# Kernel optimization log

Hardware: AMD Instinct MI355X
Metric: run time of the kernel (lower is better)

The kernel has to match this reference:

```python
import jax, jax.numpy as jnp
import numpy as np

EMB = 1280
MD = 200
N = 20000
E = 200000
LN_EPS = 1e-5


def _layer_norm(x, g, b):
    mu = jnp.mean(x, axis=-1, keepdims=True)
    var = jnp.mean((x - mu) ** 2, axis=-1, keepdims=True)
    return (x - mu) * jax.lax.rsqrt(var + LN_EPS) * g + b


def _gat_conv(x, edge_index, edge_attr, W, We, a_src, a_dst, a_edge, bias, heads, C):
    """PyG GATConv (bias-free lin, edge_dim, add_self_loops with fill='mean')."""
    n = x.shape[0]
    src, dst = edge_index[0], edge_index[1]
    # self-loop edge_attr = mean of incoming edge_attr per dst node (0 if none)
    cnt = jax.ops.segment_sum(jnp.ones((edge_attr.shape[0],), x.dtype), dst, n)
    s = jax.ops.segment_sum(edge_attr, dst, n)
    loop_attr = jnp.where(cnt[:, None] > 0, s / jnp.maximum(cnt, 1.0)[:, None], 0.0)
    loop = jnp.arange(n)
    src = jnp.concatenate([src, loop])
    dst = jnp.concatenate([dst, loop])
    ea = jnp.concatenate([edge_attr, loop_attr], axis=0)
    h = (x @ W).reshape(n, heads, C)                      # [N,H,C]
    al_s = jnp.einsum('nhc,hc->nh', h, a_src)
    al_d = jnp.einsum('nhc,hc->nh', h, a_dst)
    eh = (ea @ We).reshape(-1, heads, C)                  # [E+N,H,C]
    al_e = jnp.einsum('ehc,hc->eh', eh, a_edge)
    alpha = jax.nn.leaky_relu(al_s[src] + al_d[dst] + al_e, 0.2)
    amax = jax.ops.segment_max(alpha, dst, n)
    amax = jnp.where(jnp.isfinite(amax), amax, 0.0)
    ex = jnp.exp(alpha - amax[dst])
    denom = jax.ops.segment_sum(ex, dst, n)
    w = ex / (denom[dst] + 1e-16)                         # segment softmax over dst
    out = jax.ops.segment_sum(h[src] * w[:, :, None], dst, n)
    return out.reshape(n, heads * C) + bias


def _forward(x, edge_index, edge_attr,
             ca_qw, ca_qb, ca_kw, ca_kb, ca_vw, ca_vb, ca_ow, ca_ob,
             g0_w, g0_ew, g0_as, g0_ad, g0_ae, g0_b, ln0_g, ln0_b,
             g1_w, g1_ew, g1_as, g1_ad, g1_ae, g1_b, ln1_g, ln1_b,
             g2_w, g2_ew, g2_as, g2_ad, g2_ae, g2_b, ln2_g, ln2_b,
             cls_w1, cls_b1, cls_w2, cls_b2):
    xe = x[:, :EMB]
    md = x[0, EMB:]
    # CrossAttention: single md vector -> K,V are [1,hidden]
    Q = xe @ ca_qw + ca_qb                                # [N,hid]
    K = md @ ca_kw + ca_kb                                # [hid]
    V = md @ ca_vw + ca_vb                                # [hid]
    scores = (Q @ K) / jnp.sqrt(jnp.asarray(Q.shape[-1], Q.dtype))  # [N]
    wts = jax.nn.softmax(scores, axis=0)[:, None]         # softmax over nodes
    attended = wts * V[None, :]                           # [N,hid]
    h = attended @ ca_ow + ca_ob + xe                     # [N,EMB]

    h = _gat_conv(h, edge_index, edge_attr, g0_w, g0_ew, g0_as, g0_ad, g0_ae, g0_b, 4, 256)
    h = jax.nn.relu(_layer_norm(h, ln0_g, ln0_b))
    h = _gat_conv(h, edge_index, edge_attr, g1_w, g1_ew, g1_as, g1_ad, g1_ae, g1_b, 4, 256)
    h = jax.nn.relu(_layer_norm(h, ln1_g, ln1_b))
    h = _gat_conv(h, edge_index, edge_attr, g2_w, g2_ew, g2_as, g2_ad, g2_ae, g2_b, 1, 256)
    h = jax.nn.relu(_layer_norm(h, ln2_g, ln2_b))

    g = jnp.mean(h, axis=0, keepdims=True)                # [1,256]
    g = jax.nn.relu(g @ cls_w1 + cls_b1)
    return g @ cls_w2 + cls_b2                            # [1,2]


def setup_inputs() -> dict:
    key = jax.random.key(0)
    ks = jax.random.split(key, 64)
    i = [0]
    def nrm(shape, scale=0.05):
        i[0] += 1
        return jax.random.normal(ks[i[0]], shape, jnp.float32) * scale
    inp = {}
    inp['x'] = nrm((N, EMB + MD), 1.0)
    inp['edge_index'] = jax.random.randint(ks[60], (2, E), 0, N, jnp.int64 if jax.config.read('jax_enable_x64') else jnp.int32)
    inp['edge_attr'] = jax.random.uniform(ks[61], (E, 1), jnp.float32)
    inp.update(ca_qw=nrm((EMB, 256)), ca_qb=jnp.zeros((256,), jnp.float32),
               ca_kw=nrm((MD, 256)), ca_kb=jnp.zeros((256,), jnp.float32),
               ca_vw=nrm((MD, 256)), ca_vb=jnp.zeros((256,), jnp.float32),
               ca_ow=nrm((256, EMB)), ca_ob=jnp.zeros((EMB,), jnp.float32))
    inp.update(g0_w=nrm((EMB, 1024)), g0_ew=nrm((1, 1024)), g0_as=nrm((4, 256)),
               g0_ad=nrm((4, 256)), g0_ae=nrm((4, 256)), g0_b=jnp.zeros((1024,), jnp.float32),
               ln0_g=jnp.ones((1024,), jnp.float32), ln0_b=jnp.zeros((1024,), jnp.float32))
    inp.update(g1_w=nrm((1024, 1024)), g1_ew=nrm((1, 1024)), g1_as=nrm((4, 256)),
               g1_ad=nrm((4, 256)), g1_ae=nrm((4, 256)), g1_b=jnp.zeros((1024,), jnp.float32),
               ln1_g=jnp.ones((1024,), jnp.float32), ln1_b=jnp.zeros((1024,), jnp.float32))
    inp.update(g2_w=nrm((1024, 256)), g2_ew=nrm((1, 256)), g2_as=nrm((1, 256)),
               g2_ad=nrm((1, 256)), g2_ae=nrm((1, 256)), g2_b=jnp.zeros((256,), jnp.float32),
               ln2_g=jnp.ones((256,), jnp.float32), ln2_b=jnp.zeros((256,), jnp.float32))
    inp.update(cls_w1=nrm((256, 128)), cls_b1=jnp.zeros((128,), jnp.float32),
               cls_w2=nrm((128, 2)), cls_b2=jnp.zeros((2,), jnp.float32))
    return inp


def reference(x, edge_index, edge_attr,
              ca_qw, ca_qb, ca_kw, ca_kb, ca_vw, ca_vb, ca_ow, ca_ob,
              g0_w, g0_ew, g0_as, g0_ad, g0_ae, g0_b, ln0_g, ln0_b,
              g1_w, g1_ew, g1_as, g1_ad, g1_ae, g1_b, ln1_g, ln1_b,
              g2_w, g2_ew, g2_as, g2_ad, g2_ae, g2_b, ln2_g, ln2_b,
              cls_w1, cls_b1, cls_w2, cls_b2):
    return _forward(x, edge_index, edge_attr,
                    ca_qw, ca_qb, ca_kw, ca_kb, ca_vw, ca_vb, ca_ow, ca_ob,
                    g0_w, g0_ew, g0_as, g0_ad, g0_ae, g0_b, ln0_g, ln0_b,
                    g1_w, g1_ew, g1_as, g1_ad, g1_ae, g1_b, ln1_g, ln1_b,
                    g2_w, g2_ew, g2_as, g2_ad, g2_ae, g2_b, ln2_g, ln2_b,
                    cls_w1, cls_b1, cls_w2, cls_b2)
```

## Files before the change

kernel.cpp:

```cpp
#include <hip/hip_runtime.h>
#include <hip/hip_bf16.h>
#include <math.h>

#define N_NODES 20000
#define N_EDGES 200000
#define XROW    1480

typedef __attribute__((ext_vector_type(8))) _Float16 f16x8;
typedef __attribute__((ext_vector_type(8))) unsigned short u16x8;
typedef __attribute__((ext_vector_type(4))) float f32x4v;

__device__ __forceinline__ float wsum(float v){
#pragma unroll
  for (int o=32;o>0;o>>=1) v += __shfl_down(v,o);
  return v;
}
__device__ __forceinline__ float wmax(float v){
#pragma unroll
  for (int o=32;o>0;o>>=1) v = fmaxf(v,__shfl_down(v,o));
  return v;
}
__device__ __forceinline__ float wsum_all(float v){
#pragma unroll
  for (int o=32;o>0;o>>=1) v += __shfl_xor(v,o);
  return v;
}
__device__ __forceinline__ float wmax_all(float v){
#pragma unroll
  for (int o=32;o>0;o>>=1) v = fmaxf(v,__shfl_xor(v,o));
  return v;
}

__device__ __forceinline__ unsigned short f2hu(float f){
  _Float16 h = (_Float16)f;
  return __builtin_bit_cast(unsigned short, h);
}
__device__ __forceinline__ float hu2f(unsigned short u){
  return (float)__builtin_bit_cast(_Float16, u);
}

__device__ __forceinline__ void async_copy16(void* lds, const void* g){
  __builtin_amdgcn_global_load_lds((const __attribute__((address_space(1))) void*)g,
                                   (__attribute__((address_space(3))) void*)lds, 16, 0, 0);
}

__global__ void edge_count_kernel(const int* __restrict__ ei, const float* __restrict__ ea,
                                  int* __restrict__ cnt, float* __restrict__ easum, int E){
  int e = blockIdx.x*256 + threadIdx.x;
  if (e >= E) return;
  int dst = ei[E + e];
  atomicAdd(&cnt[dst], 1);
  atomicAdd(&easum[dst], ea[e]);
}

__launch_bounds__(1024)
__global__ void scan_kernel(const int* __restrict__ cnt, const float* __restrict__ easum,
                            int* __restrict__ off, float* __restrict__ loop_attr, int n){
  __shared__ int buf[1024];
  const int PER = (N_NODES + 1023)/1024;
  int t = threadIdx.x;
  int base = t*PER;
  int local[PER];
  int s = 0;
#pragma unroll
  for (int k=0;k<PER;k++){
    int i = base + k;
    int v = (i<n)? cnt[i] : 0;
    local[k] = v;
    s += v;
  }
  buf[t] = s;
  __syncthreads();
  for (int d2=1; d2<1024; d2<<=1){
    int tv = (t>=d2)? buf[t-d2] : 0;
    __syncthreads();
    buf[t] += tv;
    __syncthreads();
  }
  int run = buf[t] - s;
#pragma unroll
  for (int k=0;k<PER;k++){
    int i = base + k;
    if (i < n){
      off[i] = run;
      int v = local[k];
      loop_attr[i] = (v>0) ? easum[i]/(float)v : 0.f;
      run += v;
    }
  }
  if (t == 1023) off[n] = buf[1023];
}

__global__ void edge_fill_kernel(const int* __restrict__ ei, const float* __restrict__ ea,
                                 const int* __restrict__ off, int* __restrict__ fill,
                                 int* __restrict__ csr_src, float* __restrict__ csr_ea, int E){
  int e = blockIdx.x*256 + threadIdx.x;
  if (e >= E) return;
  int dst = ei[E + e];
  int pos = off[dst] + atomicAdd(&fill[dst], 1);
  csr_src[pos] = ei[e];
  csr_ea[pos]  = ea[e];
}

__global__ void wt_f16_kernel(const float* __restrict__ W, int K, int N,
                              unsigned short* __restrict__ Wt){
  __shared__ float tile[32][33];
  int k0 = blockIdx.x*32, n0 = blockIdx.y*32;
  int tx = threadIdx.x & 31, ty = threadIdx.x >> 5;
  for (int r=ty; r<32; r+=8) tile[r][tx] = W[(size_t)(k0+r)*N + n0+tx];
  __syncthreads();
  for (int r=ty; r<32; r+=8){
    float w = tile[tx][r];
    Wt[(size_t)(n0+r)*K + k0+tx] = f2hu(w);
  }
}

__global__ void kv_kernel(const float* __restrict__ x,
                          const float* __restrict__ kw, const float* __restrict__ kb,
                          const float* __restrict__ vw, const float* __restrict__ vb,
                          float* __restrict__ Kv, float* __restrict__ Vv){
  int j = threadIdx.x;
  float ka = kb[j], va = vb[j];
  for (int k=0;k<200;k++){
    float m = x[1280+k];
    ka = fmaf(m, kw[k*256+j], ka);
    va = fmaf(m, vw[k*256+j], va);
  }
  Kv[j]=ka; Vv[j]=va;
}

__global__ void qkvo_kernel(const float* __restrict__ qw, const float* __restrict__ ow,
                            const float* __restrict__ Kv, const float* __restrict__ Vv,
                            float* __restrict__ qK, float* __restrict__ Vo){
  int idx = blockIdx.x*256 + threadIdx.x;
  if (idx < 1280){
    float a=0;
    for (int j=0;j<256;j++) a = fmaf(qw[idx*256+j], Kv[j], a);
    qK[idx]=a;
  } else if (idx < 2560){
    int j = idx-1280;
    float a=0;
    for (int i=0;i<256;i++) a = fmaf(Vv[i], ow[(size_t)i*1280+j], a);
    Vo[j]=a;
  }
}

__global__ void obw_kernel(const float* __restrict__ ob, const float* __restrict__ Vo,
                           const float* __restrict__ W, float* __restrict__ obW, float* __restrict__ VoW){
  int j = blockIdx.x*256 + threadIdx.x;
  float a=0,b=0;
  for (int i=0;i<1280;i++){
    float w = W[(size_t)i*1024+j];
    a = fmaf(ob[i], w, a);
    b = fmaf(Vo[i], w, b);
  }
  obW[j]=a; VoW[j]=b;
}

__launch_bounds__(256)
__global__ void xh_scores_kernel(const float* __restrict__ x, const float* __restrict__ qK,
                                 unsigned short* __restrict__ xh, float* __restrict__ scores, int n){
  __shared__ float qs[1280];
  int t = threadIdx.x;
  for (int i=t;i<1280;i+=256) qs[i]=qK[i];
  __syncthreads();
  int wid = t>>6, lane = t&63;
  int node = blockIdx.x*4 + wid;
  if (node >= n) return;
  const float* xr = x + (size_t)node*XROW;
  unsigned short* orow = xh + (size_t)node*1280;
  float acc = 0.f;
#pragma unroll
  for (int it=0; it<5; it++){
    int c4 = it*64 + lane;
    float4 v = *(const float4*)(xr + c4*4);
    ushort4 o;
    o.x = f2hu(v.x); o.y = f2hu(v.y); o.z = f2hu(v.z); o.w = f2hu(v.w);
    *(ushort4*)(orow + c4*4) = o;
    acc = fmaf(v.x, qs[c4*4+0], acc);
    acc = fmaf(v.y, qs[c4*4+1], acc);
    acc = fmaf(v.z, qs[c4*4+2], acc);
    acc = fmaf(v.w, qs[c4*4+3], acc);
  }
  acc = wsum(acc);
  if (lane==0) scores[node] = acc;
}

__launch_bounds__(1024)
__global__ void softmax_nodes(const float* __restrict__ scores, float* __restrict__ wts, int n){
  __shared__ float red[16];
  int t = threadIdx.x, lane=t&63, wid=t>>6;
  float m = -INFINITY;
  for (int i=t;i<n;i+=1024) m = fmaxf(m, scores[i]);
  m = wmax(m);
  if (lane==0) red[wid]=m;
  __syncthreads();
  if (t==0){ float r=red[0]; for (int k=1;k<16;k++) r=fmaxf(r,red[k]); red[0]=r; }
  __syncthreads();
  float M = red[0];
  __syncthreads();
  float z=0;
  for (int i=t;i<n;i+=1024) z += __expf((scores[i]-M)*(1.f/16.f));
  z = wsum(z);
  if (lane==0) red[wid]=z;
  __syncthreads();
  if (t==0){ float r=0; for (int k=0;k<16;k++) r+=red[k]; red[0]=r; }
  __syncthreads();
  float invZ = 1.f/red[0];
  for (int i=t;i<n;i+=1024) wts[i] = __expf((scores[i]-M)*(1.f/16.f))*invZ;
}

__launch_bounds__(512,2)
__global__ void gemm256_f16(const unsigned short* __restrict__ A,
                            const unsigned short* __restrict__ B,
                            unsigned short* __restrict__ C, int M, int N, int K,
                            const float* __restrict__ addCol,
                            const float* __restrict__ vCol,
                            const float* __restrict__ wRow,
                            const float* __restrict__ a_src,
                            const float* __restrict__ a_dst,
                            float* __restrict__ als,
                            float* __restrict__ ald,
                            const float* __restrict__ We,
                            const float* __restrict__ a_edge,
                            float* __restrict__ we)
{
  __shared__ short lds[2*32768];

  const int ntc = N >> 8;
  const int sh  = (ntc==4)?2:((ntc==2)?1:0);
  const int g   = blockIdx.y >> sh;
  const int nt  = blockIdx.y & (ntc - 1);
  const int band = blockIdx.x + (g << 3);
  if (band * 256 >= M) return;

  const int t = threadIdx.x;
  const int w = t>>6, l = t&63;
  const int bm = band*256, bn = nt*256;
  const int wrh = w>>2;
  const int wcl = (w&3)*64;
  const int q4 = l>>4, m16 = l&15;

  f32x4v acc[8][4];
#pragma unroll
  for (int i=0;i<8;i++)
#pragma unroll
    for (int j=0;j<4;j++) acc[i][j] = (f32x4v){0.f,0.f,0.f,0.f};

  const unsigned short *pA00,*pA01,*pA10,*pA11,*pB00,*pB01,*pB10,*pB11;
  int lA00,lA01,lA10,lA11,lB00,lB01,lB10,lB11;
  {
#pragma unroll
    for (int half=0; half<2; half++){
#pragma unroll
      for (int q=0; q<2; q++){
        int p  = (w*2+q)*64 + l;
        int r  = p>>3, pc = p&7;
        int kc = (pc ^ (r&7))*8;
        int rowA = bm + half*128 + r; if (rowA > M-1) rowA = M-1;
        int rowB = bn + half*128 + r;
        const unsigned short* ap = A + (size_t)rowA*K + kc;
        const unsigned short* bp = B + (size_t)rowB*K + kc;
        int la = half*8192 + (w*2+q)*512;
        int lb = 16384 + la;
        if (half==0 && q==0){ pA00=ap; pB00=bp; lA00=la; lB00=lb; }
        if (half==0 && q==1){ pA01=ap; pB01=bp; lA01=la; lB01=lb; }
        if (half==1 && q==0){ pA10=ap; pB10=bp; lA10=la; lB10=lb; }
        if (half==1 && q==1){ pA11=ap; pB11=bp; lA11=la; lB11=lb; }
      }
    }
  }

  const int nk = K >> 6;

  {
    short* b0 = lds;
    async_copy16(b0 + lA00, pA00); async_copy16(b0 + lA01, pA01);
    async_copy16(b0 + lA10, pA10); async_copy16(b0 + lA11, pA11);
    async_copy16(b0 + lB00, pB00); async_copy16(b0 + lB01, pB01);
    async_copy16(b0 + lB10, pB10); async_copy16(b0 + lB11, pB11);
    asm volatile("s_waitcnt vmcnt(0)" ::: "memory");
    __builtin_amdgcn_sched_barrier(0);
    __builtin_amdgcn_s_barrier();
    __builtin_amdgcn_sched_barrier(0);
  }

  for (int kt = 0; kt < nk; ++kt){
    short* cur = lds + (kt&1)*32768;
    short* nxt = lds + ((kt+1)&1)*32768;
    const bool pre = (kt+1 < nk);
    const size_t kofs = (size_t)(kt+1)*64;

    f16x8 bf[4];
#pragma unroll
    for (int ph = 0; ph < 4; ++ph){
      const int ks = ph >> 1, ih = ph & 1;
      const int c  = ks*4 + q4;
      f16x8 af[4];
#pragma unroll
      for (int ii=0; ii<4; ii++){
        int rl = (ih*4+ii)*16 + m16;
        af[ii] = *(const f16x8*)&cur[ wrh*8192 + rl*64 + ((c ^ (rl&7))*8) ];
      }
      if (ih == 0){
#pragma unroll
        for (int j=0;j<4;j++){
          int rb = wcl + j*16 + m16;
          bf[j] = *(const f16x8*)&cur[ 16384 + rb*64 + ((c ^ (rb&7))*8) ];
        }
      }
      if (pre){
        if (ph == 0){
          async_copy16(nxt + lA00, pA00 + kofs); async_copy16(nxt + lA01, pA01 + kofs);
          async_copy16(nxt + lA10, pA10 + kofs); async_copy16(nxt + lA11, pA11 + kofs);
        } else if (ph == 1){
          async_copy16(nxt + lB00, pB00 + kofs); async_copy16(nxt + lB01, pB01 + kofs);
          async_copy16(nxt + lB10, pB10 + kofs); async_copy16(nxt + lB11, pB11 + kofs);
        }
      }
      __builtin_amdgcn_sched_barrier(0);
      __builtin_amdgcn_s_barrier();
      asm volatile("s_waitcnt lgkmcnt(0)" ::: "memory");
      __builtin_amdgcn_sched_barrier(0);

      __builtin_amdgcn_s_setprio(1);
#pragma unroll
      for (int ii=0; ii<4; ii++)
#pragma unroll
        for (int j=0; j<4; j++)
          acc[ih*4+ii][j] = __builtin_amdgcn_mfma_f32_16x16x32_f16(af[ii], bf[j], acc[ih*4+ii][j], 0,0,0);
      __builtin_amdgcn_s_setprio(0);
      __builtin_amdgcn_sched_barrier(0);
      if (ph == 3){
        asm volatile("s_waitcnt vmcnt(0)" ::: "memory");
        __builtin_amdgcn_sched_barrier(0);
      }
      __builtin_amdgcn_s_barrier();
      __builtin_amdgcn_sched_barrier(0);
    }
  }

  __syncthreads();
  float* sred = (float*)lds;
  float* dred = sred + 1024;
  const int bandc = w & 3;

  float asv[4], adv[4];
#pragma unroll
  for (int j=0;j<4;j++){
    int n = bn + wcl + j*16 + m16;
    asv[j] = a_src[n];
    adv[j] = a_dst[n];
  }
#pragma unroll
  for (int i=0;i<8;i++){
#pragma unroll
    for (int r=0;r<4;r++){
      int rloc = wrh*128 + i*16 + q4*4 + r;
      int m = bm + rloc;
      float wrow = addCol ? wRow[m < M ? m : M-1] : 0.f;
      float vj[4];
#pragma unroll
      for (int j=0;j<4;j++){
        int n = bn + wcl + j*16 + m16;
        float v = acc[i][j][r];
        if (addCol) v += addCol[n] + wrow*vCol[n];
        vj[j] = v;
      }
      if (m < M){
        unsigned short* crow = C + (size_t)m*N;
#pragma unroll
        for (int j=0;j<4;j++) crow[bn + wcl + j*16 + m16] = f2hu(vj[j]);
      }
      float s = vj[0]*asv[0] + vj[1]*asv[1] + vj[2]*asv[2] + vj[3]*asv[3];
      float d = vj[0]*adv[0] + vj[1]*adv[1] + vj[2]*adv[2] + vj[3]*adv[3];
#pragma unroll
      for (int o=1;o<16;o<<=1){ s += __shfl_xor(s,o); d += __shfl_xor(d,o); }
      if (m16 == 0){
        sred[bandc*256 + rloc] = s;
        dred[bandc*256 + rloc] = d;
      }
    }
  }
  __syncthreads();
  if (t < 256){
    int m = bm + t;
    if (m < M){
      float s = sred[t] + sred[256+t] + sred[512+t] + sred[768+t];
      float d = dred[t] + dred[256+t] + dred[512+t] + dred[768+t];
      als[(size_t)m*ntc + nt] = s;
      ald[(size_t)m*ntc + nt] = d;
    }
  }
  if (band == 0 && nt == 0 && w < ntc){
    float4 a = ((const float4*)(We + w*256))[l];
    float4 b = ((const float4*)(a_edge + w*256))[l];
    float v = a.x*b.x + a.y*b.y + a.z*b.z + a.w*b.w;
    v = wsum(v);
    if (l==0) we[w]=v;
  }
}

__launch_bounds__(256)
__global__ void gemm_f16(const unsigned short* __restrict__ A,
                         const unsigned short* __restrict__ B,
                         unsigned short* __restrict__ C, int M, int N, int K,
                         const float* __restrict__ addCol,
                         const float* __restrict__ vCol,
                         const float* __restrict__ wRow,
                         const float* __restrict__ a_src,
                         const float* __restrict__ a_dst,
                         float* __restrict__ alsp,
                         float* __restrict__ aldp)
{
  __shared__ short lds[2*2*128*64];

  const int ntc = N >> 7;
  const int sh  = __popc(ntc - 1);
  const int g   = blockIdx.y >> sh;
  const int nt  = blockIdx.y & (ntc - 1);
  const int band = blockIdx.x + (g << 3);
  if (band * 128 >= M) return;

  const int t = threadIdx.x;
  const int w = t>>6, l = t&63;
  const int bm = band*128, bn = nt*128;
  const int wr = (w>>1)*64, wc = (w&1)*64;
  const int half = w & 1;

  f32x4v acc[4][4];
#pragma unroll
  for (int i=0;i<4;i++)
#pragma unroll
    for (int j=0;j<4;j++) acc[i][j] = (f32x4v){0.f,0.f,0.f,0.f};

  const unsigned short* Ap[4]; const unsigned short* Bp[4];
  int ldsOff[4];
#pragma unroll
  for (int q=0;q<4;q++){
    int p  = (w*4+q)*64 + l;
    int r  = p>>3, pc = p&7;
    int kc = (pc ^ (r&7))*8;
    int rowA = bm + r; if (rowA > M-1) rowA = M-1;
    Ap[q] = A + (size_t)rowA*K + kc;
    Bp[q] = B + (size_t)(bn+r)*K + kc;
    ldsOff[q] = (w*4+q)*64*8;
  }

  const int nsteps = K >> 6;

#pragma unroll
  for (int q=0;q<4;q++) async_copy16(lds + ldsOff[q],        Ap[q]);
#pragma unroll
  for (int q=0;q<4;q++) async_copy16(lds + 8192 + ldsOff[q], Bp[q]);

  const int q4 = l>>4, m16 = l&15;

  for (int ks0=0; ks0<nsteps; ++ks0){
    short* curb = lds + (ks0&1)*16384;

    if (ks0+1 < nsteps){
      short* nxt = lds + ((ks0+1)&1)*16384;
      const int k0n = (ks0+1)*64;
#pragma unroll
      for (int q=0;q<4;q++) async_copy16(nxt + ldsOff[q],        Ap[q] + k0n);
#pragma unroll
      for (int q=0;q<4;q++) async_copy16(nxt + 8192 + ldsOff[q], Bp[q] + k0n);
      asm volatile("s_waitcnt vmcnt(8)" ::: "memory");
    } else {
      asm volatile("s_waitcnt vmcnt(0)" ::: "memory");
    }
    __builtin_amdgcn_sched_barrier(0);
    __builtin_amdgcn_s_barrier();
    __builtin_amdgcn_sched_barrier(0);

    __builtin_amdgcn_s_setprio(1);
#pragma unroll
    for (int ks=0; ks<2; ks++){
      f16x8 af[4], bf[4];
      const int c = ks*4 + q4;
#pragma unroll
      for (int i=0;i<4;i++){
        int ra = wr + i*16 + m16;
        af[i] = *(const f16x8*)&curb[ra*64 + ((c ^ (ra&7))*8)];
        int rb = wc + i*16 + m16;
        bf[i] = *(const f16x8*)&curb[8192 + rb*64 + ((c ^ (rb&7))*8)];
      }
#pragma unroll
      for (int i=0;i<4;i++)
#pragma unroll
        for (int j=0;j<4;j++)
          acc[i][j] = __builtin_amdgcn_mfma_f32_16x16x32_f16(af[i], bf[j], acc[i][j], 0,0,0);
    }
    __builtin_amdgcn_s_setprio(0);
    __builtin_amdgcn_sched_barrier(0);
    __builtin_amdgcn_s_barrier();
    __builtin_amdgcn_sched_barrier(0);
  }

  float* sred = (float*)lds;
  float* dred = sred + 256;
  float asv[4], adv[4];
#pragma unroll
  for (int j=0;j<4;j++){
    int n = bn + wc + j*16 + m16;
    asv[j] = a_src[n];
    adv[j] = a_dst[n];
  }
#pragma unroll
  for (int i=0;i<4;i++){
#pragma unroll
    for (int r=0;r<4;r++){
      int rloc = wr + i*16 + q4*4 + r;
      int m = bm + rloc;
      float wrow = addCol ? wRow[m < M ? m : M-1] : 0.f;
      float vj[4];
#pragma unroll
      for (int j=0;j<4;j++){
        int n = bn + wc + j*16 + m16;
        float v = acc[i][j][r];
        if (addCol) v += addCol[n] + wrow*vCol[n];
        vj[j] = v;
      }
      if (m < M){
        unsigned short* crow = C + (size_t)m*N;
#pragma unroll
        for (int j=0;j<4;j++) crow[bn + wc + j*16 + m16] = f2hu(vj[j]);
      }
      float s = vj[0]*asv[0] + vj[1]*asv[1] + vj[2]*asv[2] + vj[3]*asv[3];
      float d = vj[0]*adv[0] + vj[1]*adv[1] + vj[2]*adv[2] + vj[3]*adv[3];
#pragma unroll
      for (int o=1;o<16;o<<=1){ s += __shfl_xor(s,o); d += __shfl_xor(d,o); }
      if (m16 == 0){
        sred[half*128 + rloc] = s;
        dred[half*128 + rloc] = d;
      }
    }
  }
  __syncthreads();
  if (t < 128){
    int m = bm + t;
    if (m < M){
      alsp[(size_t)nt*M + m] = sred[t] + sred[128+t];
      aldp[(size_t)nt*M + m] = dred[t] + dred[128+t];
    }
  }
}

__global__ void als_combine(const float* __restrict__ alsp, const float* __restrict__ aldp,
                            float* __restrict__ als, float* __restrict__ ald, int M, int H,
                            const float* __restrict__ We, const float* __restrict__ a_edge,
                            float* __restrict__ we){
  if (blockIdx.x == 0){
    int wid = threadIdx.x>>6, lane = threadIdx.x&63;
    if (wid < H){
      const float4* w4 = (const float4*)(We + wid*256);
      const float4* a4 = (const float4*)(a_edge + wid*256);
      float4 a = w4[lane], b = a4[lane];
      float v = a.x*b.x + a.y*b.y + a.z*b.z + a.w*b.w;
      v = wsum(v);
      if (lane==0) we[wid]=v;
    }
  }
  int idx = blockIdx.x*256 + threadIdx.x;
  if (idx >= M*H) return;
  int m = idx / H, hh = idx - m*H;
  als[idx] = alsp[(size_t)(2*hh)*M + m] + alsp[(size_t)(2*hh+1)*M + m];
  ald[idx] = aldp[(size_t)(2*hh)*M + m] + aldp[(size_t)(2*hh+1)*M + m];
}

template<int H>
__launch_bounds__(256)
__global__ void gat_agg_ln_wave(const unsigned short* __restrict__ hmat,
                           const float* __restrict__ als, const float* __restrict__ ald,
                           const int* __restrict__ off, const int* __restrict__ csr_src,
                           const float* __restrict__ csr_ea, const float* __restrict__ loop_attr,
                           const float* __restrict__ we,
                           const float* __restrict__ bias,
                           const float* __restrict__ ln_g, const float* __restrict__ ln_b,
                           float* __restrict__ outf, unsigned short* __restrict__ outb, int n)
{
  constexpr int OUT = 256*H;
  constexpr int CPL = OUT/64;
  const int wv = threadIdx.x>>6, lane = threadIdx.x&63;
  const int i = blockIdx.x*4 + wv;
  __shared__ float wbuf_s[4][64*H];
  __shared__ int   sbuf_s[4][64];
  if (i >= n) return;
  float* wbuf = wbuf_s[wv];
  int*   sbuf = sbuf_s[wv];

  const int begin = off[i];
  const int deg   = off[i+1]-begin;
  const int S     = deg + 1;

  float aldi[H], wei[H];
#pragma unroll
  for (int hh=0;hh<H;hh++){ aldi[hh]=ald[(size_t)i*H+hh]; wei[hh]=we[hh]; }
  const float lea = loop_attr[i];

  const int head = (lane*CPL) >> 8;
  const int c0   = lane*CPL;
  float acc[CPL];
#pragma unroll
  for (int c=0;c<CPL;c++) acc[c]=0.f;

  if (S <= 64){
    int src = i; float ev = lea;
    if (lane < deg){ src = csr_src[begin+lane]; ev = csr_ea[begin+lane]; }
    const bool act = lane < S;
    sbuf[lane] = src;

    if constexpr (CPL==16){
      u16x8 a0r0,a0r1,a1r0,a1r1;
      {
        const unsigned short* r0p = hmat + (size_t)sbuf[0]*OUT + c0;
        a0r0 = *(const u16x8*)r0p; a0r1 = *(const u16x8*)(r0p+8);
        a1r0 = a0r0; a1r1 = a0r1;
        if (S > 1){
          const unsigned short* r1p = hmat + (size_t)sbuf[1]*OUT + c0;
          a1r0 = *(const u16x8*)r1p; a1r1 = *(const u16x8*)(r1p+8);
        }
      }
      float a[H];
#pragma unroll
      for (int hh=0;hh<H;hh++){
        float v = als[(size_t)src*H+hh] + aldi[hh] + ev*wei[hh];
        a[hh] = v>0.f ? v : 0.2f*v;
      }
#pragma unroll
      for (int hh=0;hh<H;hh++){
        float M = wmax_all(act ? a[hh] : -INFINITY);
        float e = act ? __expf(a[hh]-M) : 0.f;
        float Z = wsum_all(e);
        wbuf[lane*H+hh] = e / (Z + 1e-16f);
      }
      int j = 0;
      for (; j+2<S; j+=2){
        u16x8 n0r0,n0r1,n1r0,n1r1;
        {
          const unsigned short* rp = hmat + (size_t)sbuf[j+2]*OUT + c0;
          n0r0 = *(const u16x8*)rp; n0r1 = *(const u16x8*)(rp+8);
          n1r0 = n0r0; n1r1 = n0r1;
          if (j+3 < S){
            const unsigned short* rq = hmat + (size_t)sbuf[j+3]*OUT + c0;
            n1r0 = *(const u16x8*)rq; n1r1 = *(const u16x8*)(rq+8);
          }
        }
        float w0 = wbuf[j*H+head], w1 = wbuf[(j+1)*H+head];
#pragma unroll
        for (int c=0;c<8;c++){
          acc[c]   = fmaf(w0, hu2f(a0r0[c]), acc[c]);
          acc[8+c] = fmaf(w0, hu2f(a0r1[c]), acc[8+c]);
        }
#pragma unroll
        for (int c=0;c<8;c++){
          acc[c]   = fmaf(w1, hu2f(a1r0[c]), acc[c]);
          acc[8+c] = fmaf(w1, hu2f(a1r1[c]), acc[8+c]);
        }
        a0r0=n0r0; a0r1=n0r1; a1r0=n1r0; a1r1=n1r1;
      }
      {
        float w0 = wbuf[j*H+head];
#pragma unroll
        for (int c=0;c<8;c++){
          acc[c]   = fmaf(w0, hu2f(a0r0[c]), acc[c]);
          acc[8+c] = fmaf(w0, hu2f(a0r1[c]), acc[8+c]);
        }
        if (j+1 < S){
          float w1 = wbuf[(j+1)*H+head];
#pragma unroll
          for (int c=0;c<8;c++){
            acc[c]   = fmaf(w1, hu2f(a1r0[c]), acc[c]);
            acc[8+c] = fmaf(w1, hu2f(a1r1[c]), acc[8+c]);
          }
        }
      }
    } else {
      ushort4 a0, a1;
      {
        a0 = *(const ushort4*)(hmat + (size_t)sbuf[0]*OUT + c0);
        a1 = a0;
        if (S > 1) a1 = *(const ushort4*)(hmat + (size_t)sbuf[1]*OUT + c0);
      }
      float a[H];
#pragma unroll
      for (int hh=0;hh<H;hh++){
        float v = als[(size_t)src*H+hh] + aldi[hh] + ev*wei[hh];
        a[hh] = v>0.f ? v : 0.2f*v;
      }
#pragma unroll
      for (int hh=0;hh<H;hh++){
        float M = wmax_all(act ? a[hh] : -INFINITY);
        float e = act ? __expf(a[hh]-M) : 0.f;
        float Z = wsum_all(e);
        wbuf[lane*H+hh] = e / (Z + 1e-16f);
      }
      int j = 0;
      for (; j+2<S; j+=2){
        ushort4 n0, n1;
        n0 = *(const ushort4*)(hmat + (size_t)sbuf[j+2]*OUT + c0);
        n1 = n0;
        if (j+3 < S) n1 = *(const ushort4*)(hmat + (size_t)sbuf[j+3]*OUT + c0);
        float w0 = wbuf[j*H+head], w1 = wbuf[(j+1)*H+head];
        acc[0]=fmaf(w0,hu2f(a0.x),acc[0]); acc[1]=fmaf(w0,hu2f(a0.y),acc[1]);
        acc[2]=fmaf(w0,hu2f(a0.z),acc[2]); acc[3]=fmaf(w0,hu2f(a0.w),acc[3]);
        acc[0]=fmaf(w1,hu2f(a1.x),acc[0]); acc[1]=fmaf(w1,hu2f(a1.y),acc[1]);
        acc[2]=fmaf(w1,hu2f(a1.z),acc[2]); acc[3]=fmaf(w1,hu2f(a1.w),acc[3]);
        a0=n0; a1=n1;
      }
      {
        float w0 = wbuf[j*H+head];
        acc[0]=fmaf(w0,hu2f(a0.x),acc[0]); acc[1]=fmaf(w0,hu2f(a0.y),acc[1]);
        acc[2]=fmaf(w0,hu2f(a0.z),acc[2]); acc[3]=fmaf(w0,hu2f(a0.w),acc[3]);
        if (j+1 < S){
          float w1 = wbuf[(j+1)*H+head];
          acc[0]=fmaf(w1,hu2f(a1.x),acc[0]); acc[1]=fmaf(w1,hu2f(a1.y),acc[1]);
          acc[2]=fmaf(w1,hu2f(a1.z),acc[2]); acc[3]=fmaf(w1,hu2f(a1.w),acc[3]);
        }
      }
    }
  } else {
    float rm[H];
#pragma unroll
    for (int hh=0;hh<H;hh++) rm[hh] = -INFINITY;
    for (int s=lane; s<S; s+=64){
      int src = (s<deg)? csr_src[begin+s] : i;
      float ev = (s<deg)? csr_ea[begin+s] : lea;
#pragma unroll
      for (int hh=0;hh<H;hh++){
        float v = als[(size_t)src*H+hh] + aldi[hh] + ev*wei[hh];
        v = v>0.f? v : 0.2f*v;
        rm[hh] = fmaxf(rm[hh], v);
      }
    }
    float M[H], es[H];
#pragma unroll
    for (int hh=0;hh<H;hh++){ M[hh]=wmax_all(rm[hh]); es[hh]=0.f; }
    for (int s=lane; s<S; s+=64){
      int src = (s<deg)? csr_src[begin+s] : i;
      float ev = (s<deg)? csr_ea[begin+s] : lea;
#pragma unroll
      for (int hh=0;hh<H;hh++){
        float v = als[(size_t)src*H+hh] + aldi[hh] + ev*wei[hh];
        v = v>0.f? v : 0.2f*v;
        es[hh] += __expf(v - M[hh]);
      }
    }
    float invZ[H];
#pragma unroll
    for (int hh=0;hh<H;hh++) invZ[hh] = 1.f/(wsum_all(es[hh]) + 1e-16f);
    for (int cb=0; cb<S; cb+=64){
      int m = min(64, S-cb);
      int s = cb + lane;
      if (s < S){
        int src = (s<deg)? csr_src[begin+s] : i;
        float ev = (s<deg)? csr_ea[begin+s] : lea;
        sbuf[lane] = src;
#pragma unroll
        for (int hh=0;hh<H;hh++){
          float v = als[(size_t)src*H+hh] + aldi[hh] + ev*wei[hh];
          v = v>0.f? v : 0.2f*v;
          wbuf[lane*H+hh] = __expf(v - M[hh]) * invZ[hh];
        }
      }
      for (int j=0;j<m;j++){
        int sj = sbuf[j];
        float wj = wbuf[j*H+head];
        const unsigned short* row = hmat + (size_t)sj*OUT + c0;
        if constexpr (CPL==16){
          u16x8 r0 = *(const u16x8*)(row);
          u16x8 r1 = *(const u16x8*)(row+8);
#pragma unroll
          for (int c=0;c<8;c++){
            acc[c]   = fmaf(wj, hu2f(r0[c]), acc[c]);
            acc[8+c] = fmaf(wj, hu2f(r1[c]), acc[8+c]);
          }
        } else {
          ushort4 r = *(const ushort4*)(row);
          acc[0]=fmaf(wj,hu2f(r.x),acc[0]); acc[1]=fmaf(wj,hu2f(r.y),acc[1]);
          acc[2]=fmaf(wj,hu2f(r.z),acc[2]); acc[3]=fmaf(wj,hu2f(r.w),acc[3]);
        }
      }
    }
  }

  float vals[CPL];
  float ls=0.f;
#pragma unroll
  for (int c=0;c<CPL;c+=4){
    float4 b4 = *(const float4*)(bias + c0 + c);
    vals[c]=acc[c]+b4.x; vals[c+1]=acc[c+1]+b4.y; vals[c+2]=acc[c+2]+b4.z; vals[c+3]=acc[c+3]+b4.w;
    ls += vals[c]+vals[c+1]+vals[c+2]+vals[c+3];
  }
  float mu = wsum_all(ls) * (1.f/OUT);
  float lv=0.f;
#pragma unroll
  for (int c=0;c<CPL;c++){ float d=vals[c]-mu; lv += d*d; }
  float inv = rsqrtf(wsum_all(lv)*(1.f/OUT) + 1e-5f);

  if (outb){
    if constexpr (CPL==16){
#pragma unroll
      for (int c=0;c<CPL;c+=8){
        u16x8 o;
#pragma unroll
        for (int k=0;k<8;k++){
          float g = ln_g[c0+c+k], b = ln_b[c0+c+k];
          o[k] = f2hu(fmaxf((vals[c+k]-mu)*inv*g + b, 0.f));
        }
        *(u16x8*)(outb + (size_t)i*OUT + c0 + c) = o;
      }
    } else {
      ushort4 o;
      o.x = f2hu(fmaxf((vals[0]-mu)*inv*ln_g[c0+0] + ln_b[c0+0], 0.f));
      o.y = f2hu(fmaxf((vals[1]-mu)*inv*ln_g[c0+1] + ln_b[c0+1], 0.f));
      o.z = f2hu(fmaxf((vals[2]-mu)*inv*ln_g[c0+2] + ln_b[c0+2], 0.f));
      o.w = f2hu(fmaxf((vals[3]-mu)*inv*ln_g[c0+3] + ln_b[c0+3], 0.f));
      *(ushort4*)(outb + (size_t)i*OUT + c0) = o;
    }
  } else {
#pragma unroll
    for (int c=0;c<CPL;c+=4){
      float4 g4 = *(const float4*)(ln_g + c0 + c);
      float4 b4 = *(const float4*)(ln_b + c0 + c);
      float4 o;
      o.x = fmaxf((vals[c+0]-mu)*inv*g4.x + b4.x, 0.f);
      o.y = fmaxf((vals[c+1]-mu)*inv*g4.y + b4.y, 0.f);
      o.z = fmaxf((vals[c+2]-mu)*inv*g4.z + b4.z, 0.f);
      o.w = fmaxf((vals[c+3]-mu)*inv*g4.w + b4.w, 0.f);
      *(float4*)(outf + (size_t)i*OUT + c0 + c) = o;
    }
  }
}

__global__ void colsum_kernel(const float* __restrict__ h2, float* __restrict__ gsum, int n){
  int c = threadIdx.x;
  float acc=0;
  for (int i=blockIdx.x;i<n;i+=gridDim.x) acc += h2[(size_t)i*256 + c];
  atomicAdd(&gsum[c], acc);
}

__launch_bounds__(128)
__global__ void cls_kernel(const float* __restrict__ gsum,
                           const float* __restrict__ w1, const float* __restrict__ b1,
                           const float* __restrict__ w2, const float* __restrict__ b2,
                           float* __restrict__ outp){
  __shared__ float g[256];
  __shared__ float hid[128];
  int t = threadIdx.x;
  g[t]     = gsum[t]    *(1.f/N_NODES);
  g[t+128] = gsum[t+128]*(1.f/N_NODES);
  __syncthreads();
  float a = b1[t];
  for (int c=0;c<256;c++) a = fmaf(g[c], w1[c*128+t], a);
  hid[t] = fmaxf(a, 0.f);
  __syncthreads();
  if (t<2){
    float o = b2[t];
    for (int j=0;j<128;j++) o = fmaf(hid[j], w2[j*2+t], o);
    outp[t] = o;
  }
}

extern "C" void kernel_launch(void* const* d_in, const int* in_sizes, int n_in,
                              void* d_out, int out_size, void* d_ws, size_t ws_size,
                              hipStream_t stream)
{
  const float* x      = (const float*)d_in[0];
  const int*   ei     = (const int*)  d_in[1];
  const float* ea     = (const float*)d_in[2];
  const float* ca_qw  = (const float*)d_in[3];
  const float* ca_kw  = (const float*)d_in[5];
  const float* ca_kb  = (const float*)d_in[6];
  const float* ca_vw  = (const float*)d_in[7];
  const float* ca_vb  = (const float*)d_in[8];
  const float* ca_ow  = (const float*)d_in[9];
  const float* ca_ob  = (const float*)d_in[10];
  const float* g0_w   = (const float*)d_in[11];
  const float* g0_ew  = (const float*)d_in[12];
  const float* g0_as  = (const float*)d_in[13];
  const float* g0_ad  = (const float*)d_in[14];
  const float* g0_ae  = (const float*)d_in[15];
  const float* g0_b   = (const float*)d_in[16];
  const float* ln0_g  = (const float*)d_in[17];
  const float* ln0_b  = (const float*)d_in[18];
  const float* g1_w   = (const float*)d_in[19];
  const float* g1_ew  = (const float*)d_in[20];
  const float* g1_as  = (const float*)d_in[21];
  const float* g1_ad  = (const float*)d_in[22];
  const float* g1_ae  = (const float*)d_in[23];
  const float* g1_b   = (const float*)d_in[24];
  const float* ln1_g  = (const float*)d_in[25];
  const float* ln1_b  = (const float*)d_in[26];
  const float* g2_w   = (const float*)d_in[27];
  const float* g2_ew  = (const float*)d_in[28];
  const float* g2_as  = (const float*)d_in[29];
  const float* g2_ad  = (const float*)d_in[30];
  const float* g2_ae  = (const float*)d_in[31];
  const float* g2_b   = (const float*)d_in[32];
  const float* ln2_g  = (const float*)d_in[33];
  const float* ln2_b  = (const float*)d_in[34];
  const float* cls_w1 = (const float*)d_in[35];
  const float* cls_b1 = (const float*)d_in[36];
  const float* cls_w2 = (const float*)d_in[37];
  const float* cls_b2 = (const float*)d_in[38];
  float* outp = (float*)d_out;

  const int N = N_NODES, E = N_EDGES;

  char* base = (char*)d_ws;
  size_t o = 0;
  auto alloc = [&](size_t bytes)->void*{
    void* p = base + o;
    o += (bytes + 255) & ~(size_t)255;
    return p;
  };
  unsigned short* hF   = (unsigned short*)alloc((size_t)N*1024*2);
  unsigned short* Af   = (unsigned short*)alloc((size_t)N*1280*2);
  float*          h2   = (float*)         alloc((size_t)N*256*4);
  unsigned short* Wt   = (unsigned short*)alloc((size_t)1280*1024*2);
  float* alsp      = (float*)alloc((size_t)8*N*4);
  float* aldp      = (float*)alloc((size_t)8*N*4);
  float* als       = (float*)alloc((size_t)2*N*4*4);
  float* ald       = als + (size_t)N*4;
  float* scores    = (float*)alloc((size_t)N*4);
  float* wts       = (float*)alloc((size_t)N*4);
  int*   cnt       = (int*)  alloc((size_t)N*4);
  float* easum     = (float*)alloc((size_t)N*4);
  int*   off       = (int*)  alloc((size_t)(N+1)*4);
  int*   fill      = (int*)  alloc((size_t)N*4);
  int*   csr_src   = (int*)  alloc((size_t)E*4);
  float* csr_ea    = (float*)alloc((size_t)E*4);
  float* loop_attr = (float*)alloc((size_t)N*4);
  float* Kv        = (float*)alloc(256*4);
  float* Vv        = (float*)alloc(256*4);
  float* qK        = (float*)alloc(1280*4);
  float* Vo        = (float*)alloc(1280*4);
  float* obW       = (float*)alloc(1024*4);
  float* VoW       = (float*)alloc(1024*4);
  float* web       = (float*)alloc(16*4);
  float* gsum      = (float*)alloc(256*4);

  hipMemsetAsync(cnt,   0, (size_t)N*4, stream);
  hipMemsetAsync(easum, 0, (size_t)N*4, stream);
  hipMemsetAsync(fill,  0, (size_t)N*4, stream);
  hipMemsetAsync(gsum,  0, 256*4,       stream);

  int eblocks = (E + 255)/256;
  edge_count_kernel<<<eblocks,256,0,stream>>>(ei, ea, cnt, easum, E);
  scan_kernel<<<1,1024,0,stream>>>(cnt, easum, off, loop_attr, N);
  edge_fill_kernel<<<eblocks,256,0,stream>>>(ei, ea, off, fill, csr_src, csr_ea, E);

  kv_kernel<<<1,256,0,stream>>>(x, ca_kw, ca_kb, ca_vw, ca_vb, Kv, Vv);
  qkvo_kernel<<<10,256,0,stream>>>(ca_qw, ca_ow, Kv, Vv, qK, Vo);
  xh_scores_kernel<<<(N+3)/4,256,0,stream>>>(x, qK, Af, scores, N);
  obw_kernel<<<4,256,0,stream>>>(ca_ob, Vo, g0_w, obW, VoW);
  softmax_nodes<<<1,1024,0,stream>>>(scores, wts, N);

  const int mTiles  = (N + 127)/128;
  const int mGroups = (mTiles + 7)/8;
  const int mT256   = (N + 255)/256;
  const int mG256   = (mT256 + 7)/8;
  const int NB4 = (N + 3)/4;

  wt_f16_kernel<<<dim3(1280/32, 1024/32),256,0,stream>>>(g0_w, 1280, 1024, Wt);
  gemm256_f16<<<dim3(8, mG256*4),512,0,stream>>>(Af, Wt, hF, N, 1024, 1280, obW, VoW, wts,
                                                 g0_as, g0_ad, als, ald, g0_ew, g0_ae, web);
  gat_agg_ln_wave<4><<<NB4,256,0,stream>>>(hF, als, ald, off, csr_src, csr_ea, loop_attr,
                                           web, g0_b, ln0_g, ln0_b, nullptr, Af, N);

  wt_f16_kernel<<<dim3(1024/32, 1024/32),256,0,stream>>>(g1_w, 1024, 1024, Wt);
  gemm256_f16<<<dim3(8, mG256*4),512,0,stream>>>(Af, Wt, hF, N, 1024, 1024, nullptr, nullptr, nullptr,
                                                 g1_as, g1_ad, als, ald, g1_ew, g1_ae, web);
  gat_agg_ln_wave<4><<<NB4,256,0,stream>>>(hF, als, ald, off, csr_src, csr_ea, loop_attr,
                                           web, g1_b, ln1_g, ln1_b, nullptr, Af, N);

  wt_f16_kernel<<<dim3(1024/32, 256/32),256,0,stream>>>(g2_w, 1024, 256, Wt);
  gemm_f16<<<dim3(8, mGroups*2),256,0,stream>>>(Af, Wt, hF, N, 256, 1024, nullptr, nullptr, nullptr,
                                                g2_as, g2_ad, alsp, aldp);
  als_combine<<<(N+255)/256,256,0,stream>>>(alsp, aldp, als, ald, N, 1, g2_ew, g2_ae, web);
  gat_agg_ln_wave<1><<<NB4,256,0,stream>>>(hF, als, ald, off, csr_src, csr_ea, loop_attr,
                                           web, g2_b, ln2_g, ln2_b, h2, nullptr, N);

  colsum_kernel<<<256,256,0,stream>>>(h2, gsum, N);
  cls_kernel<<<1,128,0,stream>>>(gsum, cls_w1, cls_b1, cls_w2, cls_b2, outp);

  (void)in_sizes; (void)n_in; (void)out_size; (void)ws_size;
}
```

Measured before the change: 901.2 us.

## Restructure GEMM prefetch pipeline and parallelize small projection kernels

The GEMM main loop now issues all next-tile async copies at the start of each K step and waits with vmcnt(8), dropping the per-phase barrier between LDS reads and MFMA. The qK product becomes wave-per-row with float4 loads and a warp reduction, spread over 20 blocks. The obW/VoW reduction is split over 10 K-chunks using atomicAdd into buffers zeroed by memsets. These changes aim to cut barrier overhead in the GEMM and raise parallelism in tiny serial kernels, but removing the mid-loop barrier could expose LDS buffer reuse races.

```diff
diff --git a/kernel.cpp b/kernel.cpp
--- a/kernel.cpp
+++ b/kernel.cpp
@@ -132,13 +132,19 @@
 __global__ void qkvo_kernel(const float* __restrict__ qw, const float* __restrict__ ow,
                             const float* __restrict__ Kv, const float* __restrict__ Vv,
                             float* __restrict__ qK, float* __restrict__ Vo){
-  int idx = blockIdx.x*256 + threadIdx.x;
-  if (idx < 1280){
-    float a=0;
-    for (int j=0;j<256;j++) a = fmaf(qw[idx*256+j], Kv[j], a);
-    qK[idx]=a;
-  } else if (idx < 2560){
-    int j = idx-1280;
+  int b = blockIdx.x;
+  if (b < 20){
+    int wv = threadIdx.x>>6, lane = threadIdx.x&63;
+    float4 k4 = ((const float4*)Kv)[lane];
+    int w0 = b*4 + wv;
+    for (int r = w0; r < 1280; r += 80){
+      float4 q = *(const float4*)(qw + (size_t)r*256 + lane*4);
+      float v = q.x*k4.x + q.y*k4.y + q.z*k4.z + q.w*k4.w;
+      v = wsum(v);
+      if (lane==0) qK[r] = v;
+    }
+  } else {
+    int j = (b-20)*256 + threadIdx.x;
     float a=0;
     for (int i=0;i<256;i++) a = fmaf(Vv[i], ow[(size_t)i*1280+j], a);
     Vo[j]=a;
@@ -148,13 +154,15 @@
 __global__ void obw_kernel(const float* __restrict__ ob, const float* __restrict__ Vo,
                            const float* __restrict__ W, float* __restrict__ obW, float* __restrict__ VoW){
   int j = blockIdx.x*256 + threadIdx.x;
+  int i0 = blockIdx.y*128;
   float a=0,b=0;
-  for (int i=0;i<1280;i++){
+  for (int i=i0;i<i0+128;i++){
     float w = W[(size_t)i*1024+j];
     a = fmaf(ob[i], w, a);
     b = fmaf(Vo[i], w, b);
   }
-  obW[j]=a; VoW[j]=b;
+  atomicAdd(&obW[j], a);
+  atomicAdd(&VoW[j], b);
 }
 
 __launch_bounds__(256)
@@ -279,17 +287,25 @@
     async_copy16(b0 + lA10, pA10); async_copy16(b0 + lA11, pA11);
     async_copy16(b0 + lB00, pB00); async_copy16(b0 + lB01, pB01);
     async_copy16(b0 + lB10, pB10); async_copy16(b0 + lB11, pB11);
-    asm volatile("s_waitcnt vmcnt(0)" ::: "memory");
+  }
+
+  for (int kt = 0; kt < nk; ++kt){
+    short* cur = lds + (kt&1)*32768;
+
+    if (kt+1 < nk){
+      short* nxt = lds + ((kt+1)&1)*32768;
+      const size_t kofs = (size_t)(kt+1)*64;
+      async_copy16(nxt + lA00, pA00 + kofs); async_copy16(nxt + lA01, pA01 + kofs);
+      async_copy16(nxt + lA10, pA10 + kofs); async_copy16(nxt + lA11, pA11 + kofs);
+      async_copy16(nxt + lB00, pB00 + kofs); async_copy16(nxt + lB01, pB01 + kofs);
+      async_copy16(nxt + lB10, pB10 + kofs); async_copy16(nxt + lB11, pB11 + kofs);
+      asm volatile("s_waitcnt vmcnt(8)" ::: "memory");
+    } else {
+      asm volatile("s_waitcnt vmcnt(0)" ::: "memory");
+    }
     __builtin_amdgcn_sched_barrier(0);
     __builtin_amdgcn_s_barrier();
     __builtin_amdgcn_sched_barrier(0);
-  }
-
-  for (int kt = 0; kt < nk; ++kt){
-    short* cur = lds + (kt&1)*32768;
-    short* nxt = lds + ((kt+1)&1)*32768;
-    const bool pre = (kt+1 < nk);
-    const size_t kofs = (size_t)(kt+1)*64;
 
     f16x8 bf[4];
 #pragma unroll
@@ -309,20 +325,8 @@
           bf[j] = *(const f16x8*)&cur[ 16384 + rb*64 + ((c ^ (rb&7))*8) ];
         }
       }
-      if (pre){
-        if (ph == 0){
-          async_copy16(nxt + lA00, pA00 + kofs); async_copy16(nxt + lA01, pA01 + kofs);
-          async_copy16(nxt + lA10, pA10 + kofs); async_copy16(nxt + lA11, pA11 + kofs);
-        } else if (ph == 1){
-          async_copy16(nxt + lB00, pB00 + kofs); async_copy16(nxt + lB01, pB01 + kofs);
-          async_copy16(nxt + lB10, pB10 + kofs); async_copy16(nxt + lB11, pB11 + kofs);
-        }
-      }
-      __builtin_amdgcn_sched_barrier(0);
-      __builtin_amdgcn_s_barrier();
       asm volatile("s_waitcnt lgkmcnt(0)" ::: "memory");
       __builtin_amdgcn_sched_barrier(0);
-
       __builtin_amdgcn_s_setprio(1);
 #pragma unroll
       for (int ii=0; ii<4; ii++)
@@ -331,10 +335,6 @@
           acc[ih*4+ii][j] = __builtin_amdgcn_mfma_f32_16x16x32_f16(af[ii], bf[j], acc[ih*4+ii][j], 0,0,0);
       __builtin_amdgcn_s_setprio(0);
       __builtin_amdgcn_sched_barrier(0);
-      if (ph == 3){
-        asm volatile("s_waitcnt vmcnt(0)" ::: "memory");
-        __builtin_amdgcn_sched_barrier(0);
-      }
       __builtin_amdgcn_s_barrier();
       __builtin_amdgcn_sched_barrier(0);
     }
@@ -946,6 +946,8 @@
   hipMemsetAsync(easum, 0, (size_t)N*4, stream);
   hipMemsetAsync(fill,  0, (size_t)N*4, stream);
   hipMemsetAsync(gsum,  0, 256*4,       stream);
+  hipMemsetAsync(obW,   0, 1024*4,      stream);
+  hipMemsetAsync(VoW,   0, 1024*4,      stream);
 
   int eblocks = (E + 255)/256;
   edge_count_kernel<<<eblocks,256,0,stream>>>(ei, ea, cnt, easum, E);
@@ -953,9 +955,9 @@
   edge_fill_kernel<<<eblocks,256,0,stream>>>(ei, ea, off, fill, csr_src, csr_ea, E);
 
   kv_kernel<<<1,256,0,stream>>>(x, ca_kw, ca_kb, ca_vw, ca_vb, Kv, Vv);
-  qkvo_kernel<<<10,256,0,stream>>>(ca_qw, ca_ow, Kv, Vv, qK, Vo);
+  qkvo_kernel<<<25,256,0,stream>>>(ca_qw, ca_ow, Kv, Vv, qK, Vo);
   xh_scores_kernel<<<(N+3)/4,256,0,stream>>>(x, qK, Af, scores, N);
-  obw_kernel<<<4,256,0,stream>>>(ca_ob, Vo, g0_w, obW, VoW);
+  obw_kernel<<<dim3(4,10),256,0,stream>>>(ca_ob, Vo, g0_w, obW, VoW);
   softmax_nodes<<<1,1024,0,stream>>>(scores, wts, N);
 
   const int mTiles  = (N + 127)/128;
```

After: 858.7 us. 4.7% less time.
